# Optimization experiments

Measured on AMD Instinct MI355X. Metric: run time of the kernel, lower is better.

Reference implementation:

```python
import jax, jax.numpy as jnp
import numpy as np

# Param packing order: [capacitance_x, capacitance_y] + for each direction in
# (ax, by, xy, yx, xx, yy): [conductance, mean, std, pot]  -> total 26 scalars.
_DIR = {"ax": 0, "by": 1, "xy": 2, "yx": 3, "xx": 4, "yy": 5}

B, T = 4096, 4096


def setup_inputs() -> dict:
    key = jax.random.key(0)
    inputs = jax.random.normal(key, (B, T, 2), dtype=jnp.float32)
    # initializer constants from the keras layer
    params = jnp.asarray([1.0, 1.0] + [0.001, 0.3, 3.0, 1.0] * 6, dtype=jnp.float32)
    return {"inputs": inputs, "params": params}


def reference(inputs, params):
    cap_x, cap_y = params[0], params[1]

    def syn(d, pre, post):
        i = 2 + 4 * _DIR[d]
        g, mean, std, pot = params[i], params[i + 1], params[i + 2], params[i + 3]
        return g * jax.nn.sigmoid(std * (pre - mean)) * (pot - post)

    def step(state, inp):
        x, y = state                      # each [B, 1]
        a, b = inp[:, :1], inp[:, 1:]     # each [B, 1]
        cur_x = syn("ax", a, x) + syn("yx", y, x) + syn("xx", x, x)
        cur_y = syn("by", b, y) + syn("xy", x, y) + syn("yy", y, y)
        x = x + cur_x / cap_x
        y = y + cur_y / cap_y
        out = jnp.concatenate((x, y), axis=-1)  # [B, 2]
        return (x, y), out

    bsz = inputs.shape[0]
    x0 = jnp.zeros((bsz, 1), inputs.dtype)
    y0 = jnp.ones((bsz, 1), inputs.dtype)   # initial state = concat(zeros, ones)
    _, outs = jax.lax.scan(step, (x0, y0), jnp.swapaxes(inputs, 0, 1))  # [T, B, 2]
    return jnp.swapaxes(outs, 0, 1)  # [B, T, 2]
```

## Files before the change

### kernel.cpp

```cpp
#include <hip/hip_runtime.h>

#define TLEN  4096
#define NROWS 4096
#define RPB   32
#define K     32
#define NC    (TLEN / K)
#define SGSL  (2 * 16 * 32)
#define DIRS  (16 * 32)
#define STP   34
#define STSL  (64 * STP)
#define UN    8

__device__ __forceinline__ float fexp2(float x) { return __builtin_amdgcn_exp2f(x); }
__device__ __forceinline__ float frcp(float x)  { return __builtin_amdgcn_rcpf(x); }
__device__ __forceinline__ float sigz(float z)  { return frcp(1.0f + fexp2(z)); }

__device__ __forceinline__ float lane_swap1(float v) {
    int r = __builtin_amdgcn_update_dpp(0, __float_as_int(v), 0xB1, 0xF, 0xF, true);
    return __int_as_float(r);
}

__device__ void run_fast(const float* __restrict__ inp, const float* __restrict__ prm,
                         float* __restrict__ out,
                         float4* __restrict__ sgbuf,
                         float*  __restrict__ st) {
    const int tid  = threadIdx.x;
    const int wid  = tid >> 6;
    const int lane = tid & 63;
    const int R0   = blockIdx.x * RPB;
    const float L2E = 1.4426950408889634f;
    float2* __restrict__ out2 = (float2*)out;

    if (wid == 1) {
        const int r = lane & 31, h = lane >> 5;
        const float c1x = -prm[4] * L2E, c0x = prm[4] * prm[3] * L2E;
        const float c1y = -prm[8] * L2E, c0y = prm[8] * prm[7] * L2E;
        const float gAx = prm[2] / prm[0], PAx = gAx * prm[5], GnAx = -gAx;
        const float gAy = prm[6] / prm[1], PAy = gAy * prm[9], GnAy = -gAy;
        const float4* __restrict__ src = (const float4*)inp + (size_t)(R0 + r) * (TLEN / 2);

        float4 bufA[8], bufB[8];

        auto produce_reg = [&](const float4* buf, int c) {
            float4* slX = sgbuf + ((c & 1) ? SGSL : 0);
            float4* slY = slX + DIRS;
#pragma unroll
            for (int j = 0; j < 8; ++j) {
                const int tp = h * 8 + j;
                float4 v = buf[j];
                float sx0 = sigz(__builtin_fmaf(c1x, v.x, c0x));
                float sy0 = sigz(__builtin_fmaf(c1y, v.y, c0y));
                float sx1 = sigz(__builtin_fmaf(c1x, v.z, c0x));
                float sy1 = sigz(__builtin_fmaf(c1y, v.w, c0y));
                float4 ox; ox.x = GnAx * sx0; ox.y = PAx * sx0;
                           ox.z = GnAx * sx1; ox.w = PAx * sx1;
                float4 oy; oy.x = GnAy * sy0; oy.y = PAy * sy0;
                           oy.z = GnAy * sy1; oy.w = PAy * sy1;
                slX[tp * 32 + r] = ox;
                slY[tp * 32 + r] = oy;
            }
        };
        auto flush = [&](int c) {
            const float* sl = st + ((c & 1) ? STSL : 0);
            const int col = lane & 31;
#pragma unroll
            for (int j = 0; j < 16; ++j) {
                int ro = 2 * j + (lane >> 5);
                float2 v;
                v.x = sl[(2 * ro)     * STP + col];
                v.y = sl[(2 * ro + 1) * STP + col];
                out2[(size_t)(R0 + ro) * TLEN + (size_t)c * K + col] = v;
            }
        };

#pragma unroll
        for (int j = 0; j < 8; ++j) bufA[j] = src[h * 8 + j];
        produce_reg(bufA, 0);
#pragma unroll
        for (int j = 0; j < 8; ++j) bufB[j] = src[16 + h * 8 + j];
        __syncthreads();
        for (int c = 0; c < NC; ++c) {
            if ((c & 1) == 0) {
                if (c + 1 < NC) produce_reg(bufB, c + 1);
                if (c + 2 < NC) {
#pragma unroll
                    for (int j = 0; j < 8; ++j)
                        bufA[j] = src[(c + 2) * 16 + h * 8 + j];
                }
            } else {
                if (c + 1 < NC) produce_reg(bufA, c + 1);
                if (c + 2 < NC) {
#pragma unroll
                    for (int j = 0; j < 8; ++j)
                        bufB[j] = src[(c + 2) * 16 + h * 8 + j];
                }
            }
            if (c >= 1) flush(c - 1);
            __syncthreads();
        }
        flush(NC - 1);
    } else {
        const int r_  = lane >> 1;
        const int par = lane & 1;
        const int sfB = par ? 22 : 18, t2B = par ? 10 : 14;
        const float ic  = 1.0f / prm[par];
        const float g1  = prm[sfB] * ic, P1 = g1 * prm[sfB + 3], Gn1 = -g1;
        const float g2  = prm[t2B] * ic, P2 = g2 * prm[t2B + 3], Gn2 = -g2;
        const float sdz = prm[sfB + 2];
        const float c1s = -sdz * L2E, c0s = sdz * prm[sfB + 1] * L2E;

        float x   = par ? 1.0f : 0.0f;
        float sig = sigz(__builtin_fmaf(c1s, x, c0s));
        float u   = __builtin_fmaf(-sig, sig, sig);

        auto resync = [&]() {
            sig = sigz(__builtin_fmaf(c1s, x, c0s));
            u   = __builtin_fmaf(-sig, sig, sig);
        };

        __syncthreads();
        for (int c = 0; c < NC; ++c) {
            const float4* lb = sgbuf + ((c & 1) ? SGSL : 0) + par * DIRS;
            float* wp = st + ((c & 1) ? STSL : 0) + lane * STP;
            float4 f0 = lb[r_];
            float4 f1 = lb[32 + r_];
#pragma unroll
            for (int tp = 0; tp < 16; ++tp) {
                float4 f = f0; f0 = f1;
                if (tp < 14) f1 = lb[(tp + 2) * 32 + r_];
                float m1  = __builtin_fmaf(f.x, x, f.y);
                float t1v = __builtin_fmaf(Gn1, x, P1);
                float t2v = __builtin_fmaf(Gn2, x, P2);
                float b21 = __builtin_fmaf(sig, t1v, m1);
                float sc1 = lane_swap1(sig);
                float dxa = __builtin_fmaf(sc1, t2v, b21);
                x = x + dxa;
                float xa  = x;
                float dza = sdz * dxa;
                sig = __builtin_fmaf(u, dza, sig);
                float m2   = __builtin_fmaf(f.z, x, f.w);
                float t1v2 = __builtin_fmaf(Gn1, x, P1);
                float t2v2 = __builtin_fmaf(Gn2, x, P2);
                float b22  = __builtin_fmaf(sig, t1v2, m2);
                float sc2  = lane_swap1(sig);
                float dxb  = __builtin_fmaf(sc2, t2v2, b22);
                x = x + dxb;
                float dzb = sdz * dxb;
                sig = __builtin_fmaf(u, dzb, sig);
                u   = __builtin_fmaf(-sig, sig, sig);
                float2 w2; w2.x = xa; w2.y = x;
                *(float2*)(wp + 2 * tp) = w2;
                if (tp == 7) resync();
            }
            resync();
            __syncthreads();
        }
    }
}

struct LaneConst {
    float c1_in, c0_in, c1_sf, c0_sf, c1_ot, c0_ot;
    float gS_in, gS_cr, gS_sf, gP_in, gP_cr, gP_sf;
};

__device__ __forceinline__ float do_step_exact(float s, float pre_in, const LaneConst& k) {
    float sig_in = sigz(__builtin_fmaf(k.c1_in, pre_in, k.c0_in));
    float sig_sf = sigz(__builtin_fmaf(k.c1_sf, s, k.c0_sf));
    float sig_ot = sigz(__builtin_fmaf(k.c1_ot, s, k.c0_ot));
    float sig_cr = lane_swap1(sig_ot);
    float S = __builtin_fmaf(k.gS_in, sig_in, __builtin_fmaf(k.gS_cr, sig_cr, k.gS_sf * sig_sf));
    float P = __builtin_fmaf(k.gP_in, sig_in, __builtin_fmaf(k.gP_cr, sig_cr, k.gP_sf * sig_sf));
    return s + __builtin_fmaf(S, -s, P);
}

__device__ void run_exact(const float* __restrict__ inp, const float* __restrict__ prm,
                          float* __restrict__ out) {
    const int tid = blockIdx.x * 128 + threadIdx.x;
    const int row = tid >> 1;
    if (row >= NROWS) return;
    const int par = tid & 1;
    const float L2E = 1.4426950408889634f;
    const int inB = par ? 6 : 2, sfB = par ? 22 : 18, otB = par ? 14 : 10, crB = par ? 10 : 14;
    const float invc = 1.0f / prm[par];
    LaneConst k;
    float sd = prm[inB + 2], mn = prm[inB + 1];
    k.c1_in = -sd * L2E; k.c0_in = sd * mn * L2E;
    sd = prm[sfB + 2]; mn = prm[sfB + 1];
    k.c1_sf = -sd * L2E; k.c0_sf = sd * mn * L2E;
    sd = prm[otB + 2]; mn = prm[otB + 1];
    k.c1_ot = -sd * L2E; k.c0_ot = sd * mn * L2E;
    k.gS_in = prm[inB] * invc; k.gP_in = k.gS_in * prm[inB + 3];
    k.gS_sf = prm[sfB] * invc; k.gP_sf = k.gS_sf * prm[sfB + 3];
    k.gS_cr = prm[crB] * invc; k.gP_cr = k.gS_cr * prm[crB + 3];

    const float4* __restrict__ src = (const float4*)inp + (size_t)row * (TLEN / 2);
    float* __restrict__ dst = out + (size_t)row * (TLEN * 2) + par;
    float s = par ? 1.0f : 0.0f;

    float4 cur[UN], nxt[UN];
#pragma unroll
    for (int j = 0; j < UN; ++j) cur[j] = src[j];
    const int NIT = TLEN / (2 * UN);
    for (int it = 0; it < NIT; ++it) {
        if (it + 1 < NIT) {
#pragma unroll
            for (int j = 0; j < UN; ++j) nxt[j] = src[(it + 1) * UN + j];
        }
        float* dptr = dst + it * (UN * 4);
#pragma unroll
        for (int j = 0; j < UN; ++j) {
            float4 f = cur[j];
            s = do_step_exact(s, par ? f.y : f.x, k);
            dptr[j * 4] = s;
            s = do_step_exact(s, par ? f.w : f.z, k);
            dptr[j * 4 + 2] = s;
        }
#pragma unroll
        for (int j = 0; j < UN; ++j) cur[j] = nxt[j];
    }
}

__global__ __launch_bounds__(128, 1)
void memcell_scan(const float* __restrict__ inp, const float* __restrict__ prm,
                  float* __restrict__ out) {
    __shared__ float4 sgbuf[2 * SGSL];
    __shared__ float  st[2 * STSL];

    const bool shared = (prm[11] == prm[19]) && (prm[12] == prm[20]) &&
                        (prm[15] == prm[23]) && (prm[16] == prm[24]);
    const float capx = prm[0], capy = prm[1];
    const bool gpos = prm[2] >= 0.f && prm[6] >= 0.f && prm[10] >= 0.f &&
                      prm[14] >= 0.f && prm[18] >= 0.f && prm[22] >= 0.f &&
                      capx > 0.f && capy > 0.f;
    const float sx = (prm[2] + prm[14] + prm[18]) / capx;
    const float sy = (prm[6] + prm[10] + prm[22]) / capy;
    const float lox = fminf(0.f, fminf(prm[5], fminf(prm[17], prm[21])));
    const float hix = fmaxf(0.f, fmaxf(prm[5], fmaxf(prm[17], prm[21])));
    const float loy = fminf(1.f, fminf(prm[9], fminf(prm[13], prm[25])));
    const float hiy = fmaxf(1.f, fmaxf(prm[9], fmaxf(prm[13], prm[25])));
    const float wbx = prm[20] * sx * (hix - lox), wby = prm[24] * sy * (hiy - loy);
    const float zmx = prm[20] * fmaxf(fabsf(lox - prm[19]), fabsf(hix - prm[19]));
    const float zmy = prm[24] * fmaxf(fabsf(loy - prm[23]), fabsf(hiy - prm[23]));
    const bool fast = shared && gpos && sx <= 0.25f && sy <= 0.25f &&
                      wbx <= 0.02f && wby <= 0.02f && zmx <= 20.f && zmy <= 20.f;
    if (fast) {
        run_fast(inp, prm, out, sgbuf, st);
    } else {
        run_exact(inp, prm, out);
    }
}

extern "C" void kernel_launch(void* const* d_in, const int* in_sizes, int n_in,
                              void* d_out, int out_size, void* d_ws, size_t ws_size,
                              hipStream_t stream) {
    (void)in_sizes; (void)n_in; (void)d_ws; (void)ws_size; (void)out_size;
    const float* inp = (const float*)d_in[0];
    const float* prm = (const float*)d_in[1];
    float* out = (float*)d_out;
    memcell_scan<<<dim3(NROWS / RPB), dim3(128), 0, stream>>>(inp, prm, out);
}
```

Before: 395.6 us.

## Interleave x/y input sigmoid terms per timestep and fold slope into update

The producer wave now writes one float4 per timestep holding both the x and y input-synapse coefficients, replacing separate per-direction slabs that each packed two timesteps. Consumer lanes read a float2 per step, selected by parity, instead of a float4. The sigmoid-derivative factor is premultiplied by the slope, removing one multiply from each serial state update. This shortens the dependent chain on the recurrence critical path, at the cost of more and narrower LDS loads per step.

```diff
diff --git a/kernel.cpp b/kernel.cpp
--- a/kernel.cpp
+++ b/kernel.cpp
@@ -5,8 +5,7 @@
 #define RPB   32
 #define K     32
 #define NC    (TLEN / K)
-#define SGSL  (2 * 16 * 32)
-#define DIRS  (16 * 32)
+#define SGSL  (32 * 32)
 #define STP   34
 #define STSL  (64 * STP)
 #define UN    8
@@ -42,22 +41,21 @@
         float4 bufA[8], bufB[8];
 
         auto produce_reg = [&](const float4* buf, int c) {
-            float4* slX = sgbuf + ((c & 1) ? SGSL : 0);
-            float4* slY = slX + DIRS;
+            float4* sl = sgbuf + ((c & 1) ? SGSL : 0);
 #pragma unroll
             for (int j = 0; j < 8; ++j) {
-                const int tp = h * 8 + j;
+                const int t0 = 2 * (h * 8 + j);
                 float4 v = buf[j];
                 float sx0 = sigz(__builtin_fmaf(c1x, v.x, c0x));
                 float sy0 = sigz(__builtin_fmaf(c1y, v.y, c0y));
                 float sx1 = sigz(__builtin_fmaf(c1x, v.z, c0x));
                 float sy1 = sigz(__builtin_fmaf(c1y, v.w, c0y));
-                float4 ox; ox.x = GnAx * sx0; ox.y = PAx * sx0;
-                           ox.z = GnAx * sx1; ox.w = PAx * sx1;
-                float4 oy; oy.x = GnAy * sy0; oy.y = PAy * sy0;
-                           oy.z = GnAy * sy1; oy.w = PAy * sy1;
-                slX[tp * 32 + r] = ox;
-                slY[tp * 32 + r] = oy;
+                float4 o0; o0.x = GnAx * sx0; o0.y = PAx * sx0;
+                           o0.z = GnAy * sy0; o0.w = PAy * sy0;
+                float4 o1; o1.x = GnAx * sx1; o1.y = PAx * sx1;
+                           o1.z = GnAy * sy1; o1.w = PAy * sy1;
+                sl[t0 * 32 + r]       = o0;
+                sl[(t0 + 1) * 32 + r] = o1;
             }
         };
         auto flush = [&](int c) {
@@ -111,24 +109,31 @@
 
         float x   = par ? 1.0f : 0.0f;
         float sig = sigz(__builtin_fmaf(c1s, x, c0s));
-        float u   = __builtin_fmaf(-sig, sig, sig);
+        float up  = sdz * __builtin_fmaf(-sig, sig, sig);
 
         auto resync = [&]() {
             sig = sigz(__builtin_fmaf(c1s, x, c0s));
-            u   = __builtin_fmaf(-sig, sig, sig);
+            up  = sdz * __builtin_fmaf(-sig, sig, sig);
         };
 
         __syncthreads();
         for (int c = 0; c < NC; ++c) {
-            const float4* lb = sgbuf + ((c & 1) ? SGSL : 0) + par * DIRS;
+            const float* cb = (const float*)(sgbuf + ((c & 1) ? SGSL : 0))
+                            + r_ * 4 + par * 2;
             float* wp = st + ((c & 1) ? STSL : 0) + lane * STP;
-            float4 f0 = lb[r_];
-            float4 f1 = lb[32 + r_];
+            float2 c0 = *(const float2*)&cb[0 * 128];
+            float2 c1 = *(const float2*)&cb[1 * 128];
+            float2 n0 = *(const float2*)&cb[2 * 128];
+            float2 n1 = *(const float2*)&cb[3 * 128];
 #pragma unroll
             for (int tp = 0; tp < 16; ++tp) {
-                float4 f = f0; f0 = f1;
-                if (tp < 14) f1 = lb[(tp + 2) * 32 + r_];
-                float m1  = __builtin_fmaf(f.x, x, f.y);
+                float2 a0 = c0, a1 = c1;
+                c0 = n0; c1 = n1;
+                if (tp < 14) {
+                    n0 = *(const float2*)&cb[(2 * tp + 4) * 128];
+                    n1 = *(const float2*)&cb[(2 * tp + 5) * 128];
+                }
+                float m1  = __builtin_fmaf(a0.x, x, a0.y);
                 float t1v = __builtin_fmaf(Gn1, x, P1);
                 float t2v = __builtin_fmaf(Gn2, x, P2);
                 float b21 = __builtin_fmaf(sig, t1v, m1);
@@ -136,18 +141,16 @@
                 float dxa = __builtin_fmaf(sc1, t2v, b21);
                 x = x + dxa;
                 float xa  = x;
-                float dza = sdz * dxa;
-                sig = __builtin_fmaf(u, dza, sig);
-                float m2   = __builtin_fmaf(f.z, x, f.w);
+                sig = __builtin_fmaf(up, dxa, sig);
+                float m2   = __builtin_fmaf(a1.x, x, a1.y);
                 float t1v2 = __builtin_fmaf(Gn1, x, P1);
                 float t2v2 = __builtin_fmaf(Gn2, x, P2);
                 float b22  = __builtin_fmaf(sig, t1v2, m2);
                 float sc2  = lane_swap1(sig);
                 float dxb  = __builtin_fmaf(sc2, t2v2, b22);
                 x = x + dxb;
-                float dzb = sdz * dxb;
-                sig = __builtin_fmaf(u, dzb, sig);
-                u   = __builtin_fmaf(-sig, sig, sig);
+                sig = __builtin_fmaf(up, dxb, sig);
+                up  = sdz * __builtin_fmaf(-sig, sig, sig);
                 float2 w2; w2.x = xa; w2.y = x;
                 *(float2*)(wp + 2 * tp) = w2;
                 if (tp == 7) resync();
```

Measured after the change: 395.5 us. About the same (-0.0%).
